# Kernel tuning notes

Hardware: AMD Instinct MI355X
Metric: run time of the kernel (lower is better)

The kernel has to match this reference:

```python
import jax, jax.numpy as jnp
import numpy as np

DIM = 64
KSZ = 3


def _conv2d(x, w, b):
    # x: (N, C, H, W), w: (O, I, 3, 3), 'same' padding
    y = jax.lax.conv_general_dilated(
        x, w, window_strides=(1, 1), padding=[(1, 1), (1, 1)],
        dimension_numbers=("NCHW", "OIHW", "NCHW"))
    return y + b[None, :, None, None]


def setup_inputs() -> dict:
    key = jax.random.key(0)
    k1, k2, k3, k4, k5 = jax.random.split(key, 5)
    b, c, t, h, w = 2, DIM, 5, 128, 128
    x = jax.random.normal(k1, (b, c, t, h, w), dtype=jnp.float32)
    # Conv3d kernels have temporal extent 1 -> equivalent 2D kernels
    w1 = jax.random.normal(k2, (DIM, DIM, 3, 3), dtype=jnp.float32) * 0.05
    b1 = jax.random.normal(k3, (DIM,), dtype=jnp.float32) * 0.05
    w2 = jax.random.normal(k4, (KSZ * KSZ, DIM, 3, 3), dtype=jnp.float32) * 0.05
    b2 = jax.random.normal(k5, (KSZ * KSZ,), dtype=jnp.float32) * 0.05
    return {"x": x, "w1": w1, "b1": b1, "w2": w2, "b2": b2}


def reference(x, w1, b1, w2, b2):
    b, c, t, h, w = x.shape
    k = KSZ
    K = t * k * k
    # Conv3d with (1,3,3) kernel == 2D conv applied per frame
    xf = x.transpose(0, 2, 1, 3, 4).reshape(b * t, c, h, w)  # (bt, c, h, w)
    y = _conv2d(xf, w1, b1)
    y = jnp.where(y >= 0, y, 0.2 * y)  # LeakyReLU(0.2)
    ker = _conv2d(y, w2, b2)  # (bt, k*k, h, w)
    # rearrange 'b (k1 k2) t h w -> b h w (t k1 k2)'
    ker = ker.reshape(b, t, k * k, h, w).transpose(0, 3, 4, 1, 2).reshape(b, h, w, K)
    ker = ker[:, None]  # (b, 1, h, w, K)
    # kernel_normalize over last dim
    ker = ker - jnp.mean(ker, axis=-1, keepdims=True) + 1.0 / K
    # replicate pad + unfold (gather kxk neighborhoods)
    pad = (k - 1) // 2
    xp = jnp.pad(xf, ((0, 0), (0, 0), (pad, pad), (pad, pad)), mode="edge")
    patches = jnp.stack(
        [xp[:, :, i:i + h, j:j + w] for i in range(k) for j in range(k)],
        axis=-1)  # (bt, c, h, w, k*k) in (k1,k2) order like F.unfold
    # '(b t) (c k1 k2) (h w) -> b c h w (t k1 k2)'
    patches = patches.reshape(b, t, c, h, w, k * k).transpose(0, 2, 3, 4, 1, 5)
    patches = patches.reshape(b, c, h, w, K)
    return jnp.sum(patches * ker, axis=-1)  # (b, c, h, w)
```

## Files before the change

kernel.cpp:

```cpp
#include <hip/hip_runtime.h>
#include <hip/hip_bf16.h>

#define HH 128
#define WW 128
#define CC 64
#define TT 5
#define HW (HH*WW)
#define NI 10

typedef __attribute__((ext_vector_type(8))) short short8;
typedef __attribute__((ext_vector_type(4))) float f32x4;

__device__ __forceinline__ float bf2f(unsigned int bits16) {
  union { unsigned int u; float f; } v; v.u = bits16 << 16; return v.f;
}
__device__ __forceinline__ unsigned short f2bf(float f) {
  __hip_bfloat16 h = __float2bfloat16(f);
  return *reinterpret_cast<unsigned short*>(&h);
}

__global__ __launch_bounds__(256) void pack_w_k(const float* __restrict__ w1,
    const float* __restrict__ w2, unsigned short* __restrict__ wb1,
    unsigned short* __restrict__ wb2) {
  int idx = blockIdx.x*256 + threadIdx.x;
  if (idx < 64*576) {
    int oc = idx / 576, rem = idx - oc*576, kk = rem >> 6, ic = rem & 63;
    wb1[idx] = f2bf(w1[(oc*64 + ic)*9 + kk]);
  }
  if (idx < 16*576) {
    int oc = idx / 576, rem = idx - oc*576, kk = rem >> 6, ic = rem & 63;
    wb2[idx] = (oc < 9) ? f2bf(w2[(oc*64 + ic)*9 + kk]) : (unsigned short)0;
  }
}

__global__ __launch_bounds__(256) void pack_x_k(const float* __restrict__ x,
    unsigned short* __restrict__ xb) {
  __shared__ unsigned short tb[128*68];
  const int tid = threadIdx.x;
  const int n = blockIdx.x >> 7, h = blockIdx.x & 127;
  const int bi = n / 5, ti = n - bi*5;
  const float* xp = x + ((size_t)bi*CC*TT + ti)*HW + (size_t)h*WW;
  for (int e = tid; e < 64*128; e += 256) {
    int ci = e >> 7, w = e & 127;
    tb[w*68 + ci] = f2bf(xp[(size_t)ci*TT*HW + w]);
  }
  __syncthreads();
  unsigned short* dst = xb + ((size_t)n*HW + (size_t)h*WW)*64;
  for (int e = tid; e < 2048; e += 256) {
    int w = e >> 4, c = e & 15;
    *(uint2*)(dst + w*64 + c*4) = *(const uint2*)(&tb[w*68 + c*4]);
  }
}

__global__ __launch_bounds__(128, 3) void conv1_mfma(
    const unsigned short* __restrict__ xb, const unsigned short* __restrict__ wb1,
    const float* __restrict__ b1, unsigned short* __restrict__ yb) {
  __shared__ unsigned short xt[180*64];
  const int tid = threadIdx.x;
  const int wave = tid >> 6, lane = tid & 63, q = lane >> 4, r = lane & 15;
  const int n = blockIdx.z >> 1, ocg = (blockIdx.z & 1) << 5;
  const int h0 = blockIdx.y << 3, w0 = blockIdx.x << 4;
  const unsigned short* xn = xb + (size_t)n*HW*64;

  for (int e = tid; e < 1440; e += 128) {
    int sp = e >> 3, c = e & 7;
    int sr = sp / 18, sc = sp - sr*18;
    int gh = h0 + sr - 1, gw = w0 + sc - 1;
    uint4 v = make_uint4(0u,0u,0u,0u);
    if (gh >= 0 && gh < HH && gw >= 0 && gw < WW)
      v = *(const uint4*)(xn + ((size_t)(gh*WW + gw))*64 + (c << 3));
    *(uint4*)(&xt[sp*64 + ((c ^ (sp & 7)) << 3)]) = v;
  }
  __syncthreads();

  f32x4 zero4 = {0.f, 0.f, 0.f, 0.f};
  f32x4 acc[4][2];
  #pragma unroll
  for (int i = 0; i < 4; ++i)
    #pragma unroll
    for (int g = 0; g < 2; ++g) acc[i][g] = zero4;

  #pragma unroll
  for (int kk = 0; kk < 9; ++kk) {
    const int dy = kk / 3, dx = kk - dy*3;
    #pragma unroll
    for (int half = 0; half < 2; ++half) {
      short8 a0 = *(const short8*)(wb1 + (size_t)(ocg +      r)*576 + kk*64 + half*32 + (q << 3));
      short8 a1 = *(const short8*)(wb1 + (size_t)(ocg + 16 + r)*576 + kk*64 + half*32 + (q << 3));
      #pragma unroll
      for (int i = 0; i < 4; ++i) {
        int sp = (wave*4 + i + dy)*18 + (r + dx);
        short8 b = *(const short8*)(&xt[sp*64 + ((((half << 2) | q) ^ (sp & 7)) << 3)]);
        acc[i][0] = __builtin_amdgcn_mfma_f32_16x16x32_bf16(a0, b, acc[i][0], 0, 0, 0);
        acc[i][1] = __builtin_amdgcn_mfma_f32_16x16x32_bf16(a1, b, acc[i][1], 0, 0, 0);
      }
    }
  }

  #pragma unroll
  for (int i = 0; i < 4; ++i) {
    int py = wave*4 + i;
    unsigned short* yp = yb + ((size_t)n*HW + (h0+py)*WW + (w0+r))*64;
    #pragma unroll
    for (int g = 0; g < 2; ++g) {
      int oc0 = ocg + g*16 + (q << 2);
      f32x4 bias = *(const f32x4*)(b1 + oc0);
      float v0 = acc[i][g][0] + bias[0]; v0 = (v0 >= 0.f) ? v0 : 0.2f*v0;
      float v1 = acc[i][g][1] + bias[1]; v1 = (v1 >= 0.f) ? v1 : 0.2f*v1;
      float v2 = acc[i][g][2] + bias[2]; v2 = (v2 >= 0.f) ? v2 : 0.2f*v2;
      float v3 = acc[i][g][3] + bias[3]; v3 = (v3 >= 0.f) ? v3 : 0.2f*v3;
      uint2 pk;
      pk.x = (unsigned int)f2bf(v0) | ((unsigned int)f2bf(v1) << 16);
      pk.y = (unsigned int)f2bf(v2) | ((unsigned int)f2bf(v3) << 16);
      *(uint2*)(yp + oc0) = pk;
    }
  }
}

__global__ __launch_bounds__(128, 3) void conv2_mfma(
    const unsigned short* __restrict__ yb, const unsigned short* __restrict__ wb2,
    const float* __restrict__ b2, float* __restrict__ ker0) {
  __shared__ unsigned short yt[180*64];
  const int tid = threadIdx.x;
  const int wave = tid >> 6, lane = tid & 63, q = lane >> 4, r = lane & 15;
  const int n = blockIdx.z;
  const int h0 = blockIdx.y << 3, w0 = blockIdx.x << 4;
  const unsigned short* yn = yb + (size_t)n*HW*64;

  for (int e = tid; e < 1440; e += 128) {
    int sp = e >> 3, c = e & 7;
    int sr = sp / 18, sc = sp - sr*18;
    int gh = h0 + sr - 1, gw = w0 + sc - 1;
    uint4 v = make_uint4(0u,0u,0u,0u);
    if (gh >= 0 && gh < HH && gw >= 0 && gw < WW)
      v = *(const uint4*)(yn + ((size_t)(gh*WW + gw))*64 + (c << 3));
    *(uint4*)(&yt[sp*64 + ((c ^ (sp & 7)) << 3)]) = v;
  }
  __syncthreads();

  f32x4 zero4 = {0.f, 0.f, 0.f, 0.f};
  f32x4 acc[4];
  #pragma unroll
  for (int i = 0; i < 4; ++i) acc[i] = zero4;

  #pragma unroll
  for (int kk = 0; kk < 9; ++kk) {
    const int dy = kk / 3, dx = kk - dy*3;
    #pragma unroll
    for (int half = 0; half < 2; ++half) {
      short8 a = *(const short8*)(wb2 + r*576 + kk*64 + half*32 + (q << 3));
      #pragma unroll
      for (int i = 0; i < 4; ++i) {
        int sp = (wave*4 + i + dy)*18 + (r + dx);
        short8 b = *(const short8*)(&yt[sp*64 + ((((half << 2) | q) ^ (sp & 7)) << 3)]);
        acc[i] = __builtin_amdgcn_mfma_f32_16x16x32_bf16(a, b, acc[i], 0, 0, 0);
      }
    }
  }

  #pragma unroll
  for (int i = 0; i < 4; ++i) {
    int py = wave*4 + i;
    #pragma unroll
    for (int t2 = 0; t2 < 4; ++t2) {
      int oc = (q << 2) + t2;
      if (oc < 9)
        ker0[((size_t)n*9 + oc)*HW + (h0+py)*WW + w0 + r] = acc[i][t2] + b2[oc];
    }
  }
}

__global__ __launch_bounds__(256, 3) void dynf_k(
    const unsigned short* __restrict__ xb, const float* __restrict__ ker0,
    float* __restrict__ out) {
  __shared__ float xs0[TT*324*4];
  __shared__ float xs1[TT*324*4];
  const int tw = threadIdx.x, th = threadIdx.y;
  const int tid = th*16 + tw;
  const int wz = blockIdx.z;
  const int bi = wz >> 3, ci0 = (wz & 7) << 3;
  const int h0 = blockIdx.y << 4, w0 = blockIdx.x << 4;
  const int pix = (h0+th)*WW + w0 + tw;

  float kv[45]; float s = 0.f;
  #pragma unroll
  for (int t5 = 0; t5 < TT; ++t5)
    #pragma unroll
    for (int kk = 0; kk < 9; ++kk) {
      float v = ker0[((size_t)(bi*TT + t5)*9 + kk)*HW + pix];
      kv[t5*9 + kk] = v; s += v;
    }
  const float m = (s - 1.f) * (1.f/45.f);
  #pragma unroll
  for (int qq = 0; qq < 45; ++qq) kv[qq] -= m;

  for (int e = tid; e < TT*324; e += 256) {
    int t5 = e / 324, sp = e - t5*324;
    int rr = sp / 18, cc = sp - rr*18;
    int gh = min(max(h0 + rr - 1, 0), HH-1);
    int gw = min(max(w0 + cc - 1, 0), WW-1);
    uint4 raw = *(const uint4*)(xb + ((size_t)(bi*TT + t5)*HW + gh*WW + gw)*64 + ci0);
    xs0[(e << 2) + 0] = bf2f(raw.x & 0xffffu);
    xs0[(e << 2) + 1] = bf2f(raw.x >> 16);
    xs0[(e << 2) + 2] = bf2f(raw.y & 0xffffu);
    xs0[(e << 2) + 3] = bf2f(raw.y >> 16);
    xs1[(e << 2) + 0] = bf2f(raw.z & 0xffffu);
    xs1[(e << 2) + 1] = bf2f(raw.z >> 16);
    xs1[(e << 2) + 2] = bf2f(raw.w & 0xffffu);
    xs1[(e << 2) + 3] = bf2f(raw.w >> 16);
  }
  __syncthreads();

  #pragma unroll
  for (int p = 0; p < 2; ++p) {
    const float* plane = p ? xs1 : xs0;
    float a0 = 0.f, a1 = 0.f, a2 = 0.f, a3 = 0.f;
    #pragma unroll
    for (int t5 = 0; t5 < TT; ++t5)
      #pragma unroll
      for (int dy = 0; dy < 3; ++dy)
        #pragma unroll
        for (int dx = 0; dx < 3; ++dx) {
          f32x4 xv = *(const f32x4*)(&plane[(t5*324 + (th+dy)*18 + (tw+dx)) << 2]);
          float k = kv[t5*9 + dy*3 + dx];
          a0 = fmaf(xv[0], k, a0); a1 = fmaf(xv[1], k, a1);
          a2 = fmaf(xv[2], k, a2); a3 = fmaf(xv[3], k, a3);
        }
    float* op = out + ((size_t)(bi*CC + ci0 + p*4))*HW + pix;
    op[0] = a0; op[HW] = a1; op[2*(size_t)HW] = a2; op[3*(size_t)HW] = a3;
  }
}

extern "C" void kernel_launch(void* const* d_in, const int* in_sizes, int n_in,
                              void* d_out, int out_size, void* d_ws, size_t ws_size,
                              hipStream_t stream) {
  const float* x  = (const float*)d_in[0];
  const float* w1 = (const float*)d_in[1];
  const float* b1 = (const float*)d_in[2];
  const float* w2 = (const float*)d_in[3];
  const float* b2 = (const float*)d_in[4];
  float* out = (float*)d_out;

  unsigned short* xb  = (unsigned short*)d_ws;
  unsigned short* yb  = xb + (size_t)NI*HW*64;
  float*          ker0 = (float*)(yb + (size_t)NI*HW*64);
  unsigned short* wb1 = (unsigned short*)(ker0 + (size_t)NI*9*HW);
  unsigned short* wb2 = wb1 + 64*576;

  pack_w_k  <<<144, 256, 0, stream>>>(w1, w2, wb1, wb2);
  pack_x_k  <<<NI*HH, 256, 0, stream>>>(x, xb);
  conv1_mfma<<<dim3(8,16,2*NI), 128, 0, stream>>>(xb, wb1, b1, yb);
  conv2_mfma<<<dim3(8,16,NI), 128, 0, stream>>>(yb, wb2, b2, ker0);
  dynf_k    <<<dim3(8,8,16), dim3(16,16), 0, stream>>>(xb, ker0, out);
}
```

Measured before the change: 156.7 us.

## Merge pack kernels, double conv block threads, split dynamic-filter channels finer

Merges the weight-packing and input-packing kernels into one launch to save a kernel launch. The two MFMA convolution kernels now use 256 threads (4 waves), each covering 2 rows instead of 4, so the same 8x16 tile is split across more waves to raise parallelism. The dynamic-filter kernel now handles 4 channels per block instead of 8, doubling the grid and halving shared memory. In exchange it reloads and renormalizes the 45 per-pixel kernel values twice as often, and the conv kernels keep less accumulation per wave.

```diff
diff --git a/kernel.cpp b/kernel.cpp
--- a/kernel.cpp
+++ b/kernel.cpp
@@ -19,25 +19,26 @@
   return *reinterpret_cast<unsigned short*>(&h);
 }
 
-__global__ __launch_bounds__(256) void pack_w_k(const float* __restrict__ w1,
-    const float* __restrict__ w2, unsigned short* __restrict__ wb1,
+__global__ __launch_bounds__(256) void pack_k(const float* __restrict__ x,
+    const float* __restrict__ w1, const float* __restrict__ w2,
+    unsigned short* __restrict__ xb, unsigned short* __restrict__ wb1,
     unsigned short* __restrict__ wb2) {
-  int idx = blockIdx.x*256 + threadIdx.x;
-  if (idx < 64*576) {
-    int oc = idx / 576, rem = idx - oc*576, kk = rem >> 6, ic = rem & 63;
-    wb1[idx] = f2bf(w1[(oc*64 + ic)*9 + kk]);
-  }
-  if (idx < 16*576) {
-    int oc = idx / 576, rem = idx - oc*576, kk = rem >> 6, ic = rem & 63;
-    wb2[idx] = (oc < 9) ? f2bf(w2[(oc*64 + ic)*9 + kk]) : (unsigned short)0;
-  }
-}
-
-__global__ __launch_bounds__(256) void pack_x_k(const float* __restrict__ x,
-    unsigned short* __restrict__ xb) {
   __shared__ unsigned short tb[128*68];
   const int tid = threadIdx.x;
-  const int n = blockIdx.x >> 7, h = blockIdx.x & 127;
+  const int bx = blockIdx.x;
+  if (bx >= NI*HH) {
+    int idx = (bx - NI*HH)*256 + tid;
+    if (idx < 64*576) {
+      int oc = idx / 576, rem = idx - oc*576, kk = rem >> 6, ic = rem & 63;
+      wb1[idx] = f2bf(w1[(oc*64 + ic)*9 + kk]);
+    }
+    if (idx < 16*576) {
+      int oc = idx / 576, rem = idx - oc*576, kk = rem >> 6, ic = rem & 63;
+      wb2[idx] = (oc < 9) ? f2bf(w2[(oc*64 + ic)*9 + kk]) : (unsigned short)0;
+    }
+    return;
+  }
+  const int n = bx >> 7, h = bx & 127;
   const int bi = n / 5, ti = n - bi*5;
   const float* xp = x + ((size_t)bi*CC*TT + ti)*HW + (size_t)h*WW;
   for (int e = tid; e < 64*128; e += 256) {
@@ -52,7 +53,7 @@
   }
 }
 
-__global__ __launch_bounds__(128, 3) void conv1_mfma(
+__global__ __launch_bounds__(256) void conv1_mfma(
     const unsigned short* __restrict__ xb, const unsigned short* __restrict__ wb1,
     const float* __restrict__ b1, unsigned short* __restrict__ yb) {
   __shared__ unsigned short xt[180*64];
@@ -62,7 +63,7 @@
   const int h0 = blockIdx.y << 3, w0 = blockIdx.x << 4;
   const unsigned short* xn = xb + (size_t)n*HW*64;
 
-  for (int e = tid; e < 1440; e += 128) {
+  for (int e = tid; e < 1440; e += 256) {
     int sp = e >> 3, c = e & 7;
     int sr = sp / 18, sc = sp - sr*18;
     int gh = h0 + sr - 1, gw = w0 + sc - 1;
@@ -74,9 +75,9 @@
   __syncthreads();
 
   f32x4 zero4 = {0.f, 0.f, 0.f, 0.f};
-  f32x4 acc[4][2];
-  #pragma unroll
-  for (int i = 0; i < 4; ++i)
+  f32x4 acc[2][2];
+  #pragma unroll
+  for (int i = 0; i < 2; ++i)
     #pragma unroll
     for (int g = 0; g < 2; ++g) acc[i][g] = zero4;
 
@@ -88,8 +89,8 @@
       short8 a0 = *(const short8*)(wb1 + (size_t)(ocg +      r)*576 + kk*64 + half*32 + (q << 3));
       short8 a1 = *(const short8*)(wb1 + (size_t)(ocg + 16 + r)*576 + kk*64 + half*32 + (q << 3));
       #pragma unroll
-      for (int i = 0; i < 4; ++i) {
-        int sp = (wave*4 + i + dy)*18 + (r + dx);
+      for (int i = 0; i < 2; ++i) {
+        int sp = (wave*2 + i + dy)*18 + (r + dx);
         short8 b = *(const short8*)(&xt[sp*64 + ((((half << 2) | q) ^ (sp & 7)) << 3)]);
         acc[i][0] = __builtin_amdgcn_mfma_f32_16x16x32_bf16(a0, b, acc[i][0], 0, 0, 0);
         acc[i][1] = __builtin_amdgcn_mfma_f32_16x16x32_bf16(a1, b, acc[i][1], 0, 0, 0);
@@ -98,8 +99,8 @@
   }
 
   #pragma unroll
-  for (int i = 0; i < 4; ++i) {
-    int py = wave*4 + i;
+  for (int i = 0; i < 2; ++i) {
+    int py = wave*2 + i;
     unsigned short* yp = yb + ((size_t)n*HW + (h0+py)*WW + (w0+r))*64;
     #pragma unroll
     for (int g = 0; g < 2; ++g) {
@@ -117,7 +118,7 @@
   }
 }
 
-__global__ __launch_bounds__(128, 3) void conv2_mfma(
+__global__ __launch_bounds__(256) void conv2_mfma(
     const unsigned short* __restrict__ yb, const unsigned short* __restrict__ wb2,
     const float* __restrict__ b2, float* __restrict__ ker0) {
   __shared__ unsigned short yt[180*64];
@@ -127,7 +128,7 @@
   const int h0 = blockIdx.y << 3, w0 = blockIdx.x << 4;
   const unsigned short* yn = yb + (size_t)n*HW*64;
 
-  for (int e = tid; e < 1440; e += 128) {
+  for (int e = tid; e < 1440; e += 256) {
     int sp = e >> 3, c = e & 7;
     int sr = sp / 18, sc = sp - sr*18;
     int gh = h0 + sr - 1, gw = w0 + sc - 1;
@@ -139,9 +140,9 @@
   __syncthreads();
 
   f32x4 zero4 = {0.f, 0.f, 0.f, 0.f};
-  f32x4 acc[4];
-  #pragma unroll
-  for (int i = 0; i < 4; ++i) acc[i] = zero4;
+  f32x4 acc[2];
+  #pragma unroll
+  for (int i = 0; i < 2; ++i) acc[i] = zero4;
 
   #pragma unroll
   for (int kk = 0; kk < 9; ++kk) {
@@ -150,8 +151,8 @@
     for (int half = 0; half < 2; ++half) {
       short8 a = *(const short8*)(wb2 + r*576 + kk*64 + half*32 + (q << 3));
       #pragma unroll
-      for (int i = 0; i < 4; ++i) {
-        int sp = (wave*4 + i + dy)*18 + (r + dx);
+      for (int i = 0; i < 2; ++i) {
+        int sp = (wave*2 + i + dy)*18 + (r + dx);
         short8 b = *(const short8*)(&yt[sp*64 + ((((half << 2) | q) ^ (sp & 7)) << 3)]);
         acc[i] = __builtin_amdgcn_mfma_f32_16x16x32_bf16(a, b, acc[i], 0, 0, 0);
       }
@@ -159,8 +160,8 @@
   }
 
   #pragma unroll
-  for (int i = 0; i < 4; ++i) {
-    int py = wave*4 + i;
+  for (int i = 0; i < 2; ++i) {
+    int py = wave*2 + i;
     #pragma unroll
     for (int t2 = 0; t2 < 4; ++t2) {
       int oc = (q << 2) + t2;
@@ -170,15 +171,14 @@
   }
 }
 
-__global__ __launch_bounds__(256, 3) void dynf_k(
+__global__ __launch_bounds__(256) void dynf_k(
     const unsigned short* __restrict__ xb, const float* __restrict__ ker0,
     float* __restrict__ out) {
-  __shared__ float xs0[TT*324*4];
-  __shared__ float xs1[TT*324*4];
+  __shared__ float xs[TT*324*4];
   const int tw = threadIdx.x, th = threadIdx.y;
   const int tid = th*16 + tw;
   const int wz = blockIdx.z;
-  const int bi = wz >> 3, ci0 = (wz & 7) << 3;
+  const int bi = wz >> 4, ci0 = (wz & 15) << 2;
   const int h0 = blockIdx.y << 4, w0 = blockIdx.x << 4;
   const int pix = (h0+th)*WW + w0 + tw;
 
@@ -199,36 +199,30 @@
     int rr = sp / 18, cc = sp - rr*18;
     int gh = min(max(h0 + rr - 1, 0), HH-1);
     int gw = min(max(w0 + cc - 1, 0), WW-1);
-    uint4 raw = *(const uint4*)(xb + ((size_t)(bi*TT + t5)*HW + gh*WW + gw)*64 + ci0);
-    xs0[(e << 2) + 0] = bf2f(raw.x & 0xffffu);
-    xs0[(e << 2) + 1] = bf2f(raw.x >> 16);
-    xs0[(e << 2) + 2] = bf2f(raw.y & 0xffffu);
-    xs0[(e << 2) + 3] = bf2f(raw.y >> 16);
-    xs1[(e << 2) + 0] = bf2f(raw.z & 0xffffu);
-    xs1[(e << 2) + 1] = bf2f(raw.z >> 16);
-    xs1[(e << 2) + 2] = bf2f(raw.w & 0xffffu);
-    xs1[(e << 2) + 3] = bf2f(raw.w >> 16);
-  }
-  __syncthreads();
-
-  #pragma unroll
-  for (int p = 0; p < 2; ++p) {
-    const float* plane = p ? xs1 : xs0;
-    float a0 = 0.f, a1 = 0.f, a2 = 0.f, a3 = 0.f;
-    #pragma unroll
-    for (int t5 = 0; t5 < TT; ++t5)
+    uint2 raw = *(const uint2*)(xb + ((size_t)(bi*TT + t5)*HW + gh*WW + gw)*64 + ci0);
+    f32x4 f;
+    f[0] = bf2f(raw.x & 0xffffu);
+    f[1] = bf2f(raw.x >> 16);
+    f[2] = bf2f(raw.y & 0xffffu);
+    f[3] = bf2f(raw.y >> 16);
+    *(f32x4*)(&xs[e << 2]) = f;
+  }
+  __syncthreads();
+
+  float a0 = 0.f, a1 = 0.f, a2 = 0.f, a3 = 0.f;
+  #pragma unroll
+  for (int t5 = 0; t5 < TT; ++t5)
+    #pragma unroll
+    for (int dy = 0; dy < 3; ++dy)
       #pragma unroll
-      for (int dy = 0; dy < 3; ++dy)
-        #pragma unroll
-        for (int dx = 0; dx < 3; ++dx) {
-          f32x4 xv = *(const f32x4*)(&plane[(t5*324 + (th+dy)*18 + (tw+dx)) << 2]);
-          float k = kv[t5*9 + dy*3 + dx];
-          a0 = fmaf(xv[0], k, a0); a1 = fmaf(xv[1], k, a1);
-          a2 = fmaf(xv[2], k, a2); a3 = fmaf(xv[3], k, a3);
-        }
-    float* op = out + ((size_t)(bi*CC + ci0 + p*4))*HW + pix;
-    op[0] = a0; op[HW] = a1; op[2*(size_t)HW] = a2; op[3*(size_t)HW] = a3;
-  }
+      for (int dx = 0; dx < 3; ++dx) {
+        f32x4 xv = *(const f32x4*)(&xs[(t5*324 + (th+dy)*18 + (tw+dx)) << 2]);
+        float k = kv[t5*9 + dy*3 + dx];
+        a0 = fmaf(xv[0], k, a0); a1 = fmaf(xv[1], k, a1);
+        a2 = fmaf(xv[2], k, a2); a3 = fmaf(xv[3], k, a3);
+      }
+  float* op = out + ((size_t)(bi*CC + ci0))*HW + pix;
+  op[0] = a0; op[HW] = a1; op[2*(size_t)HW] = a2; op[3*(size_t)HW] = a3;
 }
 
 extern "C" void kernel_launch(void* const* d_in, const int* in_sizes, int n_in,
@@ -247,9 +241,8 @@
   unsigned short* wb1 = (unsigned short*)(ker0 + (size_t)NI*9*HW);
   unsigned short* wb2 = wb1 + 64*576;
 
-  pack_w_k  <<<144, 256, 0, stream>>>(w1, w2, wb1, wb2);
-  pack_x_k  <<<NI*HH, 256, 0, stream>>>(x, xb);
-  conv1_mfma<<<dim3(8,16,2*NI), 128, 0, stream>>>(xb, wb1, b1, yb);
-  conv2_mfma<<<dim3(8,16,NI), 128, 0, stream>>>(yb, wb2, b2, ker0);
-  dynf_k    <<<dim3(8,8,16), dim3(16,16), 0, stream>>>(xb, ker0, out);
-}
+  pack_k    <<<NI*HH + 144, 256, 0, stream>>>(x, w1, w2, xb, wb1, wb2);
+  conv1_mfma<<<dim3(8,16,2*NI), 256, 0, stream>>>(xb, wb1, b1, yb);
+  conv2_mfma<<<dim3(8,16,NI), 256, 0, stream>>>(yb, wb2, b2, ker0);
+  dynf_k    <<<dim3(8,8,32), dim3(16,16), 0, stream>>>(xb, ker0, out);
+}
```

Result: slower. 181.0 us (+15.6%).
